# Kernel tuning notes

Hardware: AMD Instinct MI355X
Metric: run time of the kernel (lower is better)

The kernel has to match this reference:

```python
import jax, jax.numpy as jnp
import numpy as np

EMBED_DIM = 1024
NUM_HEADS = 16
HEAD_DIM = EMBED_DIM // NUM_HEADS


def setup_inputs() -> dict:
    key = jax.random.key(0)
    k_x, k_wqkv, k_bqkv, k_wout, k_bout = jax.random.split(key, 5)
    B, T, C = 4, 2048, EMBED_DIM
    bound_qkv = 1.0 / np.sqrt(C)
    bound_out = 1.0 / np.sqrt(C)
    return {
        "x": jax.random.normal(k_x, (B, T, C), dtype=jnp.float32),
        # nn.Linear stores weight as [out, in]; we keep that convention.
        "w_qkv": jax.random.uniform(k_wqkv, (3 * C, C), jnp.float32, -bound_qkv, bound_qkv),
        "b_qkv": jax.random.uniform(k_bqkv, (3 * C,), jnp.float32, -bound_qkv, bound_qkv),
        "w_out": jax.random.uniform(k_wout, (C, C), jnp.float32, -bound_out, bound_out),
        "b_out": jax.random.uniform(k_bout, (C,), jnp.float32, -bound_out, bound_out),
    }


def reference(x, w_qkv, b_qkv, w_out, b_out):
    B, T, C = x.shape
    H, D = NUM_HEADS, HEAD_DIM
    qkv = x @ w_qkv.T + b_qkv                     # [B, T, 3C]
    qkv = qkv.reshape(B, T, 3, H, D)
    q = jnp.transpose(qkv[:, :, 0], (0, 2, 1, 3))  # [B, H, T, D]
    k = jnp.transpose(qkv[:, :, 1], (0, 2, 1, 3))
    v = jnp.transpose(qkv[:, :, 2], (0, 2, 1, 3))
    att = jnp.einsum('bhqd,bhkd->bhqk', q, k) / jnp.sqrt(jnp.float32(D))
    causal = jnp.tril(jnp.ones((T, T), dtype=bool))
    att = jnp.where(causal[None, None], att, -jnp.inf)
    att = jax.nn.softmax(att, axis=-1)
    # dropout p=0.0 (eval-mode identity)
    out = jnp.einsum('bhqk,bhkd->bhqd', att, v)    # [B, H, T, D]
    out = jnp.transpose(out, (0, 2, 1, 3)).reshape(B, T, C)
    return out @ w_out.T + b_out
```

## Files before the change

### kernel.cpp

```cpp
#include <hip/hip_runtime.h>
#include <hip/hip_bf16.h>


#define B_ 4
#define T_ 2048
#define C_ 1024
#define H_ 16
#define D_ 64
#define M_ (B_*T_)

#define SCALE_LOG2 0.18033688f

typedef __attribute__((ext_vector_type(8))) short short8;
typedef __attribute__((ext_vector_type(4))) float f32x4;
typedef __attribute__((ext_vector_type(16))) float f32x16;

static __device__ __forceinline__ ushort f2bf(float f) {
  __hip_bfloat16 b = __float2bfloat16(f);
  ushort u; __builtin_memcpy(&u, &b, 2); return u;
}

static __device__ __forceinline__ void ld16(const void* g, void* l) {
  __builtin_amdgcn_global_load_lds((const __attribute__((address_space(1))) void*)g,
                                   (__attribute__((address_space(3))) void*)l, 16, 0, 0);
}

static __device__ __forceinline__ f32x4 mfma16(short8 a, short8 b, f32x4 c) {
  return __builtin_amdgcn_mfma_f32_16x16x32_bf16(a, b, c, 0, 0, 0);
}
static __device__ __forceinline__ f32x16 mfma32(short8 a, short8 b, f32x16 c) {
  return __builtin_amdgcn_mfma_f32_32x32x16_bf16(a, b, c, 0, 0, 0);
}

static __device__ __forceinline__ float pair_max(float x) {
  return fmaxf(x, __shfl_xor(x, 32));
}
static __device__ __forceinline__ float pair_sum(float x) {
  return x + __shfl_xor(x, 32);
}

__global__ void cvt_bf16(const float* __restrict__ in, ushort* __restrict__ out, int n4) {
  int i = blockIdx.x * blockDim.x + threadIdx.x;
  int st = gridDim.x * blockDim.x;
  for (; i < n4; i += st) {
    float4 v = ((const float4*)in)[i];
    ushort4 o;
    o.x = f2bf(v.x); o.y = f2bf(v.y); o.z = f2bf(v.z); o.w = f2bf(v.w);
    ((ushort4*)out)[i] = o;
  }
}

template<int MODE>
__global__ __launch_bounds__(256) void gemm_bt(
    const ushort* __restrict__ A, const ushort* __restrict__ Bm,
    const float* __restrict__ bias, int K,
    ushort* __restrict__ q, ushort* __restrict__ kk, ushort* __restrict__ vt,
    float* __restrict__ outF)
{
  __shared__ ushort Al[2][128*32];
  __shared__ ushort Bl[2][128*32];
  const int tid = threadIdx.x;
  const int lane = tid & 63;
  const int w = tid >> 6;
  const int wr = w >> 1, wc = w & 1;
  const int l15 = lane & 15, lhi = lane >> 4;
  const long i0 = (long)blockIdx.y * 128;
  const long j0 = (long)blockIdx.x * 128;

  const int gsw = (lhi ^ ((l15 >> 1) & 3)) * 8;

  auto STAGE = [&](int buf, int k0) {
    int c = tid;
    int row = c >> 2, gs = (c & 3) ^ ((row >> 1) & 3);
    ld16((const char*)A  + ((i0 + row) * K + k0 + gs * 8) * 2, (char*)&Al[buf][0] + c * 16);
    ld16((const char*)Bm + ((j0 + row) * K + k0 + gs * 8) * 2, (char*)&Bl[buf][0] + c * 16);
    c = tid + 256;
    row = c >> 2; gs = (c & 3) ^ ((row >> 1) & 3);
    ld16((const char*)A  + ((i0 + row) * K + k0 + gs * 8) * 2, (char*)&Al[buf][0] + c * 16);
    ld16((const char*)Bm + ((j0 + row) * K + k0 + gs * 8) * 2, (char*)&Bl[buf][0] + c * 16);
  };

  f32x4 acc[4][4] = {};
  const int nsteps = K >> 5;

  STAGE(0, 0);
  STAGE(1, 32);
  int cur = 0;

  for (int t = 0; t < nsteps; t++) {
    if (t + 1 < nsteps) { asm volatile("s_waitcnt vmcnt(4)" ::: "memory"); }
    else                { asm volatile("s_waitcnt vmcnt(0)" ::: "memory"); }
    __builtin_amdgcn_s_barrier();
    __builtin_amdgcn_sched_barrier(0);

    short8 af[4], bf[4];
#pragma unroll
    for (int m = 0; m < 4; m++) af[m] = *(const short8*)&Al[cur][(wr*64 + m*16 + l15)*32 + gsw];
#pragma unroll
    for (int n = 0; n < 4; n++) bf[n] = *(const short8*)&Bl[cur][(wc*64 + n*16 + l15)*32 + gsw];
    __builtin_amdgcn_s_setprio(1);
#pragma unroll
    for (int m = 0; m < 4; m++)
#pragma unroll
      for (int n = 0; n < 4; n++)
        acc[m][n] = mfma16(af[m], bf[n], acc[m][n]);
    __builtin_amdgcn_s_setprio(0);

    __builtin_amdgcn_s_barrier();
    __builtin_amdgcn_sched_barrier(0);
    if (t + 2 < nsteps) STAGE(cur, (t + 2) * 32);
    cur ^= 1;
  }

#pragma unroll
  for (int m = 0; m < 4; m++) {
#pragma unroll
    for (int n = 0; n < 4; n++) {
#pragma unroll
      for (int r = 0; r < 4; r++) {
        long i = i0 + wr*64 + m*16 + lhi*4 + r;
        int  j = (int)j0 + wc*64 + n*16 + l15;
        float v = acc[m][n][r] + bias[j];
        if (MODE == 0) {
          int b = (int)(i >> 11), t = (int)(i & 2047);
          int sel = j >> 10, cc = j & 1023;
          int h = cc >> 6, d = cc & 63;
          long bh = (long)b * H_ + h;
          if (sel == 0)      q [(bh*T_ + t)*D_ + d] = f2bf(v * SCALE_LOG2);
          else if (sel == 1) kk[(bh*T_ + t)*D_ + d] = f2bf(v);
          else               vt[(bh*D_ + d)*T_ + t] = f2bf(v);
        } else {
          outF[i * C_ + j] = v;
        }
      }
    }
  }
}

#define PSTR 20

static __device__ __forceinline__ void softmax_pack32(
    f32x16& sc, float& m, float& lp, f32x16 (&o)[2],
    int q0, int kvbase, int l31, int hi, uint* __restrict__ P)
{
  float sv[16];
  const bool needmask = (kvbase + 31 > q0);
#pragma unroll
  for (int r = 0; r < 16; r++) {
    float xv = sc[r];
    if (needmask) {
      int kv = kvbase + (r & 3) + 8 * (r >> 2) + 4 * hi;
      if (kv > q0 + l31) xv = -1e30f;
    }
    sv[r] = xv;
  }
  float p0 = fmaxf(fmaxf(sv[0], sv[1]),  fmaxf(sv[2], sv[3]));
  float p1 = fmaxf(fmaxf(sv[4], sv[5]),  fmaxf(sv[6], sv[7]));
  float p2 = fmaxf(fmaxf(sv[8], sv[9]),  fmaxf(sv[10], sv[11]));
  float p3 = fmaxf(fmaxf(sv[12], sv[13]), fmaxf(sv[14], sv[15]));
  float pm = fmaxf(fmaxf(p0, p1), fmaxf(p2, p3));
  float rowm = pair_max(pm);
  float nm = fmaxf(m, rowm);
  float alpha = __builtin_amdgcn_exp2f(m - nm);
  m = nm;
  lp *= alpha;
#pragma unroll
  for (int dt = 0; dt < 2; dt++)
#pragma unroll
    for (int r = 0; r < 16; r++) o[dt][r] *= alpha;
  float s = 0.f;
#pragma unroll
  for (int r = 0; r < 16; r++) {
    float p = __builtin_amdgcn_exp2f(sv[r] - m);
    sv[r] = p;
    s += p;
  }
  lp += s;
  uint W[8];
#pragma unroll
  for (int r = 0; r < 8; r++)
    asm("v_cvt_pk_bf16_f32 %0, %1, %2" : "=v"(W[r]) : "v"(sv[2*r]), "v"(sv[2*r+1]));
#pragma unroll
  for (int r2 = 0; r2 < 4; r2++) {
    uint2 pr; pr.x = W[2*r2]; pr.y = W[2*r2 + 1];
    *(uint2*)&P[l31 * PSTR + r2*4 + 2*hi] = pr;
  }
}

__global__ __launch_bounds__(256, 2) void attn_k(
    const ushort* __restrict__ Q, const ushort* __restrict__ K,
    const ushort* __restrict__ V, ushort* __restrict__ AO)
{
  __shared__ ushort Kt[2][128*64];
  __shared__ ushort Vt[2][64*128];
  __shared__ uint P2[4][32 * PSTR];
  const int tid = threadIdx.x;
  const int lane = tid & 63;
  const int w = tid >> 6;
  const int l31 = lane & 31, hi = lane >> 5;
  const int bb = blockIdx.x;
  const int head = bb & 63;
  const int i = bb >> 6;
  const int J = (i < 4) ? i : 11 - i;
  const int nst = 16 - J;
  const int q0a = 128 * J + 32 * w;
  const int q0b = 2016 - 128 * J - 32 * w;

  const ushort* Qb = Q + (size_t)head * T_ * D_;
  const ushort* Kb = K + (size_t)head * T_ * D_;
  const ushort* Vb = V + (size_t)head * D_ * T_;

  auto STAGE = [&](int buf, int kv0s) {
#pragma unroll
    for (int hb = 0; hb < 4; hb++) {
      int slot = tid + hb * 256;
      int krow = slot >> 3, kg = slot & 7, kgs = kg ^ (krow & 7);
      ld16((const char*)Kb + ((size_t)(kv0s + krow) * D_ + kgs * 8) * 2,
           (char*)&Kt[buf][0] + slot * 16);
      int vrow = slot >> 4, vg = slot & 15, vgs = vg ^ (vrow & 15);
      ld16((const char*)Vb + ((size_t)vrow * T_ + kv0s + vgs * 8) * 2,
           (char*)&Vt[buf][0] + slot * 16);
    }
  };

  short8 qfa[4], qfb[4];
#pragma unroll
  for (int s = 0; s < 4; s++) {
    qfa[s] = *(const short8*)&Qb[(q0a + l31) * D_ + s*16 + hi*8];
    qfb[s] = *(const short8*)&Qb[(q0b + l31) * D_ + s*16 + hi*8];
  }

  f32x16 oa[2] = {}, ob[2] = {};
  float ma = -1e30f, la = 0.f, mb = -1e30f, lb = 0.f;

  STAGE(0, 0);
  STAGE(1, 128);
  int cur = 0;
  uint* P = &P2[w][0];

  for (int t = 0; t < nst; t++) {
    const int kv0 = t * 128;
    if (t + 1 < nst) { asm volatile("s_waitcnt vmcnt(8)" ::: "memory"); }
    else             { asm volatile("s_waitcnt vmcnt(0)" ::: "memory"); }
    __builtin_amdgcn_s_barrier();
    __builtin_amdgcn_sched_barrier(0);

#pragma unroll
    for (int c = 0; c < 4; c++) {
      const int kvc = kv0 + 32 * c;
      const bool act_b = (kvc <= q0b + 31);
      const bool act_a = (kvc <= q0a + 31);
      if (act_b) {
        short8 kf[4];
#pragma unroll
        for (int s = 0; s < 4; s++) {
          const int row = c*32 + l31;
          kf[s] = *(const short8*)&Kt[cur][row*64 + (((2*s + hi) ^ (row & 7)) << 3)];
        }
        short8 vf[2][2];
#pragma unroll
        for (int sl = 0; sl < 2; sl++)
#pragma unroll
          for (int dt = 0; dt < 2; dt++) {
            const int row = dt*32 + l31;
            const int u = c*4 + sl*2 + hi;
            vf[sl][dt] = *(const short8*)
                &Vt[cur][row*128 + ((u ^ (row & 15)) << 3)];
          }

        {
          f32x16 scb = {};
          __builtin_amdgcn_s_setprio(1);
#pragma unroll
          for (int s = 0; s < 4; s++) scb = mfma32(kf[s], qfb[s], scb);
          __builtin_amdgcn_s_setprio(0);
          softmax_pack32(scb, mb, lb, ob, q0b, kvc, l31, hi, P);
          asm volatile("s_waitcnt lgkmcnt(0)" ::: "memory");
          __builtin_amdgcn_sched_barrier(0);
          short8 pf[2];
#pragma unroll
          for (int sl = 0; sl < 2; sl++) {
            uint4 pw = *(const uint4*)&P[l31 * PSTR + sl*8 + hi*4];
            __builtin_memcpy(&pf[sl], &pw, 16);
          }
          __builtin_amdgcn_s_setprio(1);
#pragma unroll
          for (int sl = 0; sl < 2; sl++)
#pragma unroll
            for (int dt = 0; dt < 2; dt++)
              ob[dt] = mfma32(vf[sl][dt], pf[sl], ob[dt]);
          __builtin_amdgcn_s_setprio(0);
          __builtin_amdgcn_sched_barrier(0);
        }
        if (act_a) {
          f32x16 sca = {};
          __builtin_amdgcn_s_setprio(1);
#pragma unroll
          for (int s = 0; s < 4; s++) sca = mfma32(kf[s], qfa[s], sca);
          __builtin_amdgcn_s_setprio(0);
          softmax_pack32(sca, ma, la, oa, q0a, kvc, l31, hi, P);
          asm volatile("s_waitcnt lgkmcnt(0)" ::: "memory");
          __builtin_amdgcn_sched_barrier(0);
          short8 pf[2];
#pragma unroll
          for (int sl = 0; sl < 2; sl++) {
            uint4 pw = *(const uint4*)&P[l31 * PSTR + sl*8 + hi*4];
            __builtin_memcpy(&pf[sl], &pw, 16);
          }
          __builtin_amdgcn_s_setprio(1);
#pragma unroll
          for (int sl = 0; sl < 2; sl++)
#pragma unroll
            for (int dt = 0; dt < 2; dt++)
              oa[dt] = mfma32(vf[sl][dt], pf[sl], oa[dt]);
          __builtin_amdgcn_s_setprio(0);
          __builtin_amdgcn_sched_barrier(0);
        }
      }
    }

    __builtin_amdgcn_s_barrier();
    __builtin_amdgcn_sched_barrier(0);
    if (t + 2 < nst) STAGE(cur, kv0 + 256);
    cur ^= 1;
  }

  const int b = head >> 4, h = head & 15;
  {
    const float invl = 1.0f / pair_sum(lb);
    const size_t rowb = (size_t)(b * T_ + q0b + l31) * C_ + h * 64;
#pragma unroll
    for (int dt = 0; dt < 2; dt++)
#pragma unroll
      for (int rg = 0; rg < 4; rg++) {
        const int d0 = dt*32 + 8*rg + 4*hi;
        ushort4 ov;
        ov.x = f2bf(ob[dt][rg*4+0] * invl);
        ov.y = f2bf(ob[dt][rg*4+1] * invl);
        ov.z = f2bf(ob[dt][rg*4+2] * invl);
        ov.w = f2bf(ob[dt][rg*4+3] * invl);
        *(ushort4*)&AO[rowb + d0] = ov;
      }
  }
  {
    const float invl = 1.0f / pair_sum(la);
    const size_t rowb = (size_t)(b * T_ + q0a + l31) * C_ + h * 64;
#pragma unroll
    for (int dt = 0; dt < 2; dt++)
#pragma unroll
      for (int rg = 0; rg < 4; rg++) {
        const int d0 = dt*32 + 8*rg + 4*hi;
        ushort4 ov;
        ov.x = f2bf(oa[dt][rg*4+0] * invl);
        ov.y = f2bf(oa[dt][rg*4+1] * invl);
        ov.z = f2bf(oa[dt][rg*4+2] * invl);
        ov.w = f2bf(oa[dt][rg*4+3] * invl);
        *(ushort4*)&AO[rowb + d0] = ov;
      }
  }
}

extern "C" void kernel_launch(void* const* d_in, const int* in_sizes, int n_in,
                              void* d_out, int out_size, void* d_ws, size_t ws_size,
                              hipStream_t stream) {
  const float* x     = (const float*)d_in[0];
  const float* w_qkv = (const float*)d_in[1];
  const float* b_qkv = (const float*)d_in[2];
  const float* w_out = (const float*)d_in[3];
  const float* b_out = (const float*)d_in[4];
  float* out = (float*)d_out;

  ushort* xb    = (ushort*)d_ws;
  ushort* wqkvb = xb    + (size_t)M_ * C_;
  ushort* woutb = wqkvb + (size_t)3 * C_ * C_;
  ushort* q     = woutb + (size_t)C_ * C_;
  ushort* kk    = q     + (size_t)M_ * C_;
  ushort* vt    = kk    + (size_t)M_ * C_;
  ushort* ao    = xb;

  cvt_bf16<<<1024, 256, 0, stream>>>(x,     xb,    (M_ * C_) / 4);
  cvt_bf16<<<512,  256, 0, stream>>>(w_qkv, wqkvb, (3 * C_ * C_) / 4);
  cvt_bf16<<<256,  256, 0, stream>>>(w_out, woutb, (C_ * C_) / 4);

  gemm_bt<0><<<dim3(3 * C_ / 128, M_ / 128), 256, 0, stream>>>(
      xb, wqkvb, b_qkv, C_, q, kk, vt, nullptr);

  attn_k<<<B_ * H_ * T_ / 256, 256, 0, stream>>>(q, kk, vt, ao);

  gemm_bt<1><<<dim3(C_ / 128, M_ / 128), 256, 0, stream>>>(
      ao, woutb, b_out, C_, nullptr, nullptr, nullptr, out);
}
```

Before: 206.5 us.

## Fuse conversion kernels, stage V-transpose epilogue via LDS, split attention blocks by row

After: 184.6 us. -10.6%, faster.

```diff
diff --git a/kernel.cpp b/kernel.cpp
--- a/kernel.cpp
+++ b/kernel.cpp
@@ -39,14 +39,22 @@
   return x + __shfl_xor(x, 32);
 }
 
-__global__ void cvt_bf16(const float* __restrict__ in, ushort* __restrict__ out, int n4) {
+__global__ void cvt3(const float* __restrict__ a, const float* __restrict__ b,
+                     const float* __restrict__ c, ushort* __restrict__ oa,
+                     ushort* __restrict__ ob, ushort* __restrict__ oc,
+                     int na, int nb, int nc) {
+  int tot = na + nb + nc;
   int i = blockIdx.x * blockDim.x + threadIdx.x;
   int st = gridDim.x * blockDim.x;
-  for (; i < n4; i += st) {
-    float4 v = ((const float4*)in)[i];
+  for (; i < tot; i += st) {
+    const float* s; ushort* d; int k = i;
+    if (k < na)            { s = a; d = oa; }
+    else if (k < na + nb)  { k -= na; s = b; d = ob; }
+    else                   { k -= na + nb; s = c; d = oc; }
+    float4 v = ((const float4*)s)[k];
     ushort4 o;
     o.x = f2bf(v.x); o.y = f2bf(v.y); o.z = f2bf(v.z); o.w = f2bf(v.w);
-    ((ushort4*)out)[i] = o;
+    ((ushort4*)d)[k] = o;
   }
 }
 
@@ -57,8 +65,7 @@
     ushort* __restrict__ q, ushort* __restrict__ kk, ushort* __restrict__ vt,
     float* __restrict__ outF)
 {
-  __shared__ ushort Al[2][128*32];
-  __shared__ ushort Bl[2][128*32];
+  __shared__ ushort SM[17408];
   const int tid = threadIdx.x;
   const int lane = tid & 63;
   const int w = tid >> 6;
@@ -72,12 +79,12 @@
   auto STAGE = [&](int buf, int k0) {
     int c = tid;
     int row = c >> 2, gs = (c & 3) ^ ((row >> 1) & 3);
-    ld16((const char*)A  + ((i0 + row) * K + k0 + gs * 8) * 2, (char*)&Al[buf][0] + c * 16);
-    ld16((const char*)Bm + ((j0 + row) * K + k0 + gs * 8) * 2, (char*)&Bl[buf][0] + c * 16);
+    ld16((const char*)A  + ((i0 + row) * K + k0 + gs * 8) * 2, (char*)SM + buf*8192 + c*16);
+    ld16((const char*)Bm + ((j0 + row) * K + k0 + gs * 8) * 2, (char*)SM + 16384 + buf*8192 + c*16);
     c = tid + 256;
     row = c >> 2; gs = (c & 3) ^ ((row >> 1) & 3);
-    ld16((const char*)A  + ((i0 + row) * K + k0 + gs * 8) * 2, (char*)&Al[buf][0] + c * 16);
-    ld16((const char*)Bm + ((j0 + row) * K + k0 + gs * 8) * 2, (char*)&Bl[buf][0] + c * 16);
+    ld16((const char*)A  + ((i0 + row) * K + k0 + gs * 8) * 2, (char*)SM + buf*8192 + c*16);
+    ld16((const char*)Bm + ((j0 + row) * K + k0 + gs * 8) * 2, (char*)SM + 16384 + buf*8192 + c*16);
   };
 
   f32x4 acc[4][4] = {};
@@ -95,9 +102,11 @@
 
     short8 af[4], bf[4];
 #pragma unroll
-    for (int m = 0; m < 4; m++) af[m] = *(const short8*)&Al[cur][(wr*64 + m*16 + l15)*32 + gsw];
-#pragma unroll
-    for (int n = 0; n < 4; n++) bf[n] = *(const short8*)&Bl[cur][(wc*64 + n*16 + l15)*32 + gsw];
+    for (int m = 0; m < 4; m++)
+      af[m] = *(const short8*)&SM[cur*4096 + (wr*64 + m*16 + l15)*32 + gsw];
+#pragma unroll
+    for (int n = 0; n < 4; n++)
+      bf[n] = *(const short8*)&SM[8192 + cur*4096 + (wc*64 + n*16 + l15)*32 + gsw];
     __builtin_amdgcn_s_setprio(1);
 #pragma unroll
     for (int m = 0; m < 4; m++)
@@ -112,25 +121,55 @@
     cur ^= 1;
   }
 
-#pragma unroll
-  for (int m = 0; m < 4; m++) {
-#pragma unroll
-    for (int n = 0; n < 4; n++) {
-#pragma unroll
-      for (int r = 0; r < 4; r++) {
-        long i = i0 + wr*64 + m*16 + lhi*4 + r;
-        int  j = (int)j0 + wc*64 + n*16 + l15;
-        float v = acc[m][n][r] + bias[j];
-        if (MODE == 0) {
-          int b = (int)(i >> 11), t = (int)(i & 2047);
-          int sel = j >> 10, cc = j & 1023;
-          int h = cc >> 6, d = cc & 63;
-          long bh = (long)b * H_ + h;
-          if (sel == 0)      q [(bh*T_ + t)*D_ + d] = f2bf(v * SCALE_LOG2);
-          else if (sel == 1) kk[(bh*T_ + t)*D_ + d] = f2bf(v);
-          else               vt[(bh*D_ + d)*T_ + t] = f2bf(v);
-        } else {
-          outF[i * C_ + j] = v;
+  if (MODE == 0 && j0 >= 2048) {
+#pragma unroll
+    for (int m = 0; m < 4; m++)
+#pragma unroll
+      for (int n = 0; n < 4; n++) {
+        const int jl = wc*64 + n*16 + l15;
+        const int tl = wr*64 + m*16 + lhi*4;
+        const float bs = bias[j0 + jl];
+        uint w0, w1;
+        asm("v_cvt_pk_bf16_f32 %0, %1, %2" : "=v"(w0)
+            : "v"(acc[m][n][0] + bs), "v"(acc[m][n][1] + bs));
+        asm("v_cvt_pk_bf16_f32 %0, %1, %2" : "=v"(w1)
+            : "v"(acc[m][n][2] + bs), "v"(acc[m][n][3] + bs));
+        uint2 pr; pr.x = w0; pr.y = w1;
+        *(uint2*)&SM[jl * 136 + tl] = pr;
+      }
+    __syncthreads();
+    const int b = (int)(i0 >> 11);
+    const int tb = (int)(i0 & 2047);
+#pragma unroll
+    for (int k2 = 0; k2 < 8; k2++) {
+      const int chunk = k2 * 256 + tid;
+      const int jl = chunk >> 4;
+      const int t0 = (chunk & 15) * 8;
+      uint4 pw = *(const uint4*)&SM[jl * 136 + t0];
+      const int cc = (int)((j0 + jl) & 1023);
+      const int h = cc >> 6, d = cc & 63;
+      *(uint4*)&vt[((size_t)(b * H_ + h) * D_ + d) * T_ + tb + t0] = pw;
+    }
+  } else {
+#pragma unroll
+    for (int m = 0; m < 4; m++) {
+#pragma unroll
+      for (int n = 0; n < 4; n++) {
+#pragma unroll
+        for (int r = 0; r < 4; r++) {
+          long i = i0 + wr*64 + m*16 + lhi*4 + r;
+          int  j = (int)j0 + wc*64 + n*16 + l15;
+          float v = acc[m][n][r] + bias[j];
+          if (MODE == 0) {
+            int b = (int)(i >> 11), t = (int)(i & 2047);
+            int cc = j & 1023;
+            int h = cc >> 6, d = cc & 63;
+            long bh = (long)b * H_ + h;
+            if (j < 1024)      q [(bh*T_ + t)*D_ + d] = f2bf(v * SCALE_LOG2);
+            else               kk[(bh*T_ + t)*D_ + d] = f2bf(v);
+          } else {
+            outF[i * C_ + j] = v;
+          }
         }
       }
     }
@@ -200,11 +239,9 @@
   const int l31 = lane & 31, hi = lane >> 5;
   const int bb = blockIdx.x;
   const int head = bb & 63;
-  const int i = bb >> 6;
-  const int J = (i < 4) ? i : 11 - i;
-  const int nst = 16 - J;
-  const int q0a = 128 * J + 32 * w;
-  const int q0b = 2016 - 128 * J - 32 * w;
+  const int rblk = 15 - (bb >> 6);
+  const int nst = rblk + 1;
+  const int q0 = 128 * rblk + 32 * w;
 
   const ushort* Qb = Q + (size_t)head * T_ * D_;
   const ushort* Kb = K + (size_t)head * T_ * D_;
@@ -223,15 +260,13 @@
     }
   };
 
-  short8 qfa[4], qfb[4];
-#pragma unroll
-  for (int s = 0; s < 4; s++) {
-    qfa[s] = *(const short8*)&Qb[(q0a + l31) * D_ + s*16 + hi*8];
-    qfb[s] = *(const short8*)&Qb[(q0b + l31) * D_ + s*16 + hi*8];
-  }
-
-  f32x16 oa[2] = {}, ob[2] = {};
-  float ma = -1e30f, la = 0.f, mb = -1e30f, lb = 0.f;
+  short8 qf[4];
+#pragma unroll
+  for (int s = 0; s < 4; s++)
+    qf[s] = *(const short8*)&Qb[(q0 + l31) * D_ + s*16 + hi*8];
+
+  f32x16 o[2] = {};
+  float m = -1e30f, lp = 0.f;
 
   STAGE(0, 0);
   STAGE(1, 128);
@@ -248,9 +283,7 @@
 #pragma unroll
     for (int c = 0; c < 4; c++) {
       const int kvc = kv0 + 32 * c;
-      const bool act_b = (kvc <= q0b + 31);
-      const bool act_a = (kvc <= q0a + 31);
-      if (act_b) {
+      if (kvc <= q0 + 31) {
         short8 kf[4];
 #pragma unroll
         for (int s = 0; s < 4; s++) {
@@ -268,54 +301,28 @@
                 &Vt[cur][row*128 + ((u ^ (row & 15)) << 3)];
           }
 
-        {
-          f32x16 scb = {};
-          __builtin_amdgcn_s_setprio(1);
-#pragma unroll
-          for (int s = 0; s < 4; s++) scb = mfma32(kf[s], qfb[s], scb);
-          __builtin_amdgcn_s_setprio(0);
-          softmax_pack32(scb, mb, lb, ob, q0b, kvc, l31, hi, P);
-          asm volatile("s_waitcnt lgkmcnt(0)" ::: "memory");
-          __builtin_amdgcn_sched_barrier(0);
-          short8 pf[2];
-#pragma unroll
-          for (int sl = 0; sl < 2; sl++) {
-            uint4 pw = *(const uint4*)&P[l31 * PSTR + sl*8 + hi*4];
-            __builtin_memcpy(&pf[sl], &pw, 16);
-          }
-          __builtin_amdgcn_s_setprio(1);
-#pragma unroll
-          for (int sl = 0; sl < 2; sl++)
-#pragma unroll
-            for (int dt = 0; dt < 2; dt++)
-              ob[dt] = mfma32(vf[sl][dt], pf[sl], ob[dt]);
-          __builtin_amdgcn_s_setprio(0);
-          __builtin_amdgcn_sched_barrier(0);
+        f32x16 sc = {};
+        __builtin_amdgcn_s_setprio(1);
+#pragma unroll
+        for (int s = 0; s < 4; s++) sc = mfma32(kf[s], qf[s], sc);
+        __builtin_amdgcn_s_setprio(0);
+        softmax_pack32(sc, m, lp, o, q0, kvc, l31, hi, P);
+        asm volatile("s_waitcnt lgkmcnt(0)" ::: "memory");
+        __builtin_amdgcn_sched_barrier(0);
+        short8 pf[2];
+#pragma unroll
+        for (int sl = 0; sl < 2; sl++) {
+          uint4 pw = *(const uint4*)&P[l31 * PSTR + sl*8 + hi*4];
+          __builtin_memcpy(&pf[sl], &pw, 16);
         }
-        if (act_a) {
-          f32x16 sca = {};
-          __builtin_amdgcn_s_setprio(1);
-#pragma unroll
-          for (int s = 0; s < 4; s++) sca = mfma32(kf[s], qfa[s], sca);
-          __builtin_amdgcn_s_setprio(0);
-          softmax_pack32(sca, ma, la, oa, q0a, kvc, l31, hi, P);
-          asm volatile("s_waitcnt lgkmcnt(0)" ::: "memory");
-          __builtin_amdgcn_sched_barrier(0);
-          short8 pf[2];
-#pragma unroll
-          for (int sl = 0; sl < 2; sl++) {
-            uint4 pw = *(const uint4*)&P[l31 * PSTR + sl*8 + hi*4];
-            __builtin_memcpy(&pf[sl], &pw, 16);
-          }
-          __builtin_amdgcn_s_setprio(1);
-#pragma unroll
-          for (int sl = 0; sl < 2; sl++)
-#pragma unroll
-            for (int dt = 0; dt < 2; dt++)
-              oa[dt] = mfma32(vf[sl][dt], pf[sl], oa[dt]);
-          __builtin_amdgcn_s_setprio(0);
-          __builtin_amdgcn_sched_barrier(0);
-        }
+        __builtin_amdgcn_s_setprio(1);
+#pragma unroll
+        for (int sl = 0; sl < 2; sl++)
+#pragma unroll
+          for (int dt = 0; dt < 2; dt++)
+            o[dt] = mfma32(vf[sl][dt], pf[sl], o[dt]);
+        __builtin_amdgcn_s_setprio(0);
+        __builtin_amdgcn_sched_barrier(0);
       }
     }
 
@@ -326,38 +333,20 @@
   }
 
   const int b = head >> 4, h = head & 15;
-  {
-    const float invl = 1.0f / pair_sum(lb);
-    const size_t rowb = (size_t)(b * T_ + q0b + l31) * C_ + h * 64;
-#pragma unroll
-    for (int dt = 0; dt < 2; dt++)
-#pragma unroll
-      for (int rg = 0; rg < 4; rg++) {
-        const int d0 = dt*32 + 8*rg + 4*hi;
-        ushort4 ov;
-        ov.x = f2bf(ob[dt][rg*4+0] * invl);
-        ov.y = f2bf(ob[dt][rg*4+1] * invl);
-        ov.z = f2bf(ob[dt][rg*4+2] * invl);
-        ov.w = f2bf(ob[dt][rg*4+3] * invl);
-        *(ushort4*)&AO[rowb + d0] = ov;
-      }
-  }
-  {
-    const float invl = 1.0f / pair_sum(la);
-    const size_t rowb = (size_t)(b * T_ + q0a + l31) * C_ + h * 64;
-#pragma unroll
-    for (int dt = 0; dt < 2; dt++)
-#pragma unroll
-      for (int rg = 0; rg < 4; rg++) {
-        const int d0 = dt*32 + 8*rg + 4*hi;
-        ushort4 ov;
-        ov.x = f2bf(oa[dt][rg*4+0] * invl);
-        ov.y = f2bf(oa[dt][rg*4+1] * invl);
-        ov.z = f2bf(oa[dt][rg*4+2] * invl);
-        ov.w = f2bf(oa[dt][rg*4+3] * invl);
-        *(ushort4*)&AO[rowb + d0] = ov;
-      }
-  }
+  const float invl = 1.0f / pair_sum(lp);
+  const size_t rowb = (size_t)(b * T_ + q0 + l31) * C_ + h * 64;
+#pragma unroll
+  for (int dt = 0; dt < 2; dt++)
+#pragma unroll
+    for (int rg = 0; rg < 4; rg++) {
+      const int d0 = dt*32 + 8*rg + 4*hi;
+      ushort4 ov;
+      ov.x = f2bf(o[dt][rg*4+0] * invl);
+      ov.y = f2bf(o[dt][rg*4+1] * invl);
+      ov.z = f2bf(o[dt][rg*4+2] * invl);
+      ov.w = f2bf(o[dt][rg*4+3] * invl);
+      *(ushort4*)&AO[rowb + d0] = ov;
+    }
 }
 
 extern "C" void kernel_launch(void* const* d_in, const int* in_sizes, int n_in,
@@ -378,14 +367,13 @@
   ushort* vt    = kk    + (size_t)M_ * C_;
   ushort* ao    = xb;
 
-  cvt_bf16<<<1024, 256, 0, stream>>>(x,     xb,    (M_ * C_) / 4);
-  cvt_bf16<<<512,  256, 0, stream>>>(w_qkv, wqkvb, (3 * C_ * C_) / 4);
-  cvt_bf16<<<256,  256, 0, stream>>>(w_out, woutb, (C_ * C_) / 4);
+  cvt3<<<2048, 256, 0, stream>>>(x, w_qkv, w_out, xb, wqkvb, woutb,
+                                 (M_ * C_) / 4, (3 * C_ * C_) / 4, (C_ * C_) / 4);
 
   gemm_bt<0><<<dim3(3 * C_ / 128, M_ / 128), 256, 0, stream>>>(
       xb, wqkvb, b_qkv, C_, q, kk, vt, nullptr);
 
-  attn_k<<<B_ * H_ * T_ / 256, 256, 0, stream>>>(q, kk, vt, ao);
+  attn_k<<<B_ * H_ * T_ / 128, 256, 0, stream>>>(q, kk, vt, ao);
 
   gemm_bt<1><<<dim3(C_ / 128, M_ / 128), 256, 0, stream>>>(
       ao, woutb, b_out, C_, nullptr, nullptr, nullptr, out);
```

## Fuse conversions, stage V-transpose via LDS, lazy softmax rescale, smaller attention tiles

Applied to the files above, without the earlier changes.

Result: faster. 175.8 us (-14.9%).

```diff
diff --git a/kernel.cpp b/kernel.cpp
--- a/kernel.cpp
+++ b/kernel.cpp
@@ -39,14 +39,22 @@
   return x + __shfl_xor(x, 32);
 }
 
-__global__ void cvt_bf16(const float* __restrict__ in, ushort* __restrict__ out, int n4) {
+__global__ void cvt3(const float* __restrict__ a, const float* __restrict__ b,
+                     const float* __restrict__ c, ushort* __restrict__ oa,
+                     ushort* __restrict__ ob, ushort* __restrict__ oc,
+                     int na, int nb, int nc) {
+  int tot = na + nb + nc;
   int i = blockIdx.x * blockDim.x + threadIdx.x;
   int st = gridDim.x * blockDim.x;
-  for (; i < n4; i += st) {
-    float4 v = ((const float4*)in)[i];
+  for (; i < tot; i += st) {
+    const float* s; ushort* d; int k = i;
+    if (k < na)            { s = a; d = oa; }
+    else if (k < na + nb)  { k -= na; s = b; d = ob; }
+    else                   { k -= na + nb; s = c; d = oc; }
+    float4 v = ((const float4*)s)[k];
     ushort4 o;
     o.x = f2bf(v.x); o.y = f2bf(v.y); o.z = f2bf(v.z); o.w = f2bf(v.w);
-    ((ushort4*)out)[i] = o;
+    ((ushort4*)d)[k] = o;
   }
 }
 
@@ -57,8 +65,7 @@
     ushort* __restrict__ q, ushort* __restrict__ kk, ushort* __restrict__ vt,
     float* __restrict__ outF)
 {
-  __shared__ ushort Al[2][128*32];
-  __shared__ ushort Bl[2][128*32];
+  __shared__ ushort SM[17408];
   const int tid = threadIdx.x;
   const int lane = tid & 63;
   const int w = tid >> 6;
@@ -72,12 +79,12 @@
   auto STAGE = [&](int buf, int k0) {
     int c = tid;
     int row = c >> 2, gs = (c & 3) ^ ((row >> 1) & 3);
-    ld16((const char*)A  + ((i0 + row) * K + k0 + gs * 8) * 2, (char*)&Al[buf][0] + c * 16);
-    ld16((const char*)Bm + ((j0 + row) * K + k0 + gs * 8) * 2, (char*)&Bl[buf][0] + c * 16);
+    ld16((const char*)A  + ((i0 + row) * K + k0 + gs * 8) * 2, (char*)SM + buf*8192 + c*16);
+    ld16((const char*)Bm + ((j0 + row) * K + k0 + gs * 8) * 2, (char*)SM + 16384 + buf*8192 + c*16);
     c = tid + 256;
     row = c >> 2; gs = (c & 3) ^ ((row >> 1) & 3);
-    ld16((const char*)A  + ((i0 + row) * K + k0 + gs * 8) * 2, (char*)&Al[buf][0] + c * 16);
-    ld16((const char*)Bm + ((j0 + row) * K + k0 + gs * 8) * 2, (char*)&Bl[buf][0] + c * 16);
+    ld16((const char*)A  + ((i0 + row) * K + k0 + gs * 8) * 2, (char*)SM + buf*8192 + c*16);
+    ld16((const char*)Bm + ((j0 + row) * K + k0 + gs * 8) * 2, (char*)SM + 16384 + buf*8192 + c*16);
   };
 
   f32x4 acc[4][4] = {};
@@ -95,9 +102,11 @@
 
     short8 af[4], bf[4];
 #pragma unroll
-    for (int m = 0; m < 4; m++) af[m] = *(const short8*)&Al[cur][(wr*64 + m*16 + l15)*32 + gsw];
-#pragma unroll
-    for (int n = 0; n < 4; n++) bf[n] = *(const short8*)&Bl[cur][(wc*64 + n*16 + l15)*32 + gsw];
+    for (int m = 0; m < 4; m++)
+      af[m] = *(const short8*)&SM[cur*4096 + (wr*64 + m*16 + l15)*32 + gsw];
+#pragma unroll
+    for (int n = 0; n < 4; n++)
+      bf[n] = *(const short8*)&SM[8192 + cur*4096 + (wc*64 + n*16 + l15)*32 + gsw];
     __builtin_amdgcn_s_setprio(1);
 #pragma unroll
     for (int m = 0; m < 4; m++)
@@ -112,25 +121,55 @@
     cur ^= 1;
   }
 
-#pragma unroll
-  for (int m = 0; m < 4; m++) {
-#pragma unroll
-    for (int n = 0; n < 4; n++) {
-#pragma unroll
-      for (int r = 0; r < 4; r++) {
-        long i = i0 + wr*64 + m*16 + lhi*4 + r;
-        int  j = (int)j0 + wc*64 + n*16 + l15;
-        float v = acc[m][n][r] + bias[j];
-        if (MODE == 0) {
-          int b = (int)(i >> 11), t = (int)(i & 2047);
-          int sel = j >> 10, cc = j & 1023;
-          int h = cc >> 6, d = cc & 63;
-          long bh = (long)b * H_ + h;
-          if (sel == 0)      q [(bh*T_ + t)*D_ + d] = f2bf(v * SCALE_LOG2);
-          else if (sel == 1) kk[(bh*T_ + t)*D_ + d] = f2bf(v);
-          else               vt[(bh*D_ + d)*T_ + t] = f2bf(v);
-        } else {
-          outF[i * C_ + j] = v;
+  if (MODE == 0 && j0 >= 2048) {
+#pragma unroll
+    for (int m = 0; m < 4; m++)
+#pragma unroll
+      for (int n = 0; n < 4; n++) {
+        const int jl = wc*64 + n*16 + l15;
+        const int tl = wr*64 + m*16 + lhi*4;
+        const float bs = bias[j0 + jl];
+        uint w0, w1;
+        asm("v_cvt_pk_bf16_f32 %0, %1, %2" : "=v"(w0)
+            : "v"(acc[m][n][0] + bs), "v"(acc[m][n][1] + bs));
+        asm("v_cvt_pk_bf16_f32 %0, %1, %2" : "=v"(w1)
+            : "v"(acc[m][n][2] + bs), "v"(acc[m][n][3] + bs));
+        uint2 pr; pr.x = w0; pr.y = w1;
+        *(uint2*)&SM[jl * 136 + tl] = pr;
+      }
+    __syncthreads();
+    const int b = (int)(i0 >> 11);
+    const int tb = (int)(i0 & 2047);
+#pragma unroll
+    for (int k2 = 0; k2 < 8; k2++) {
+      const int chunk = k2 * 256 + tid;
+      const int jl = chunk >> 4;
+      const int t0 = (chunk & 15) * 8;
+      uint4 pw = *(const uint4*)&SM[jl * 136 + t0];
+      const int cc = (int)((j0 + jl) & 1023);
+      const int h = cc >> 6, d = cc & 63;
+      *(uint4*)&vt[((size_t)(b * H_ + h) * D_ + d) * T_ + tb + t0] = pw;
+    }
+  } else {
+#pragma unroll
+    for (int m = 0; m < 4; m++) {
+#pragma unroll
+      for (int n = 0; n < 4; n++) {
+#pragma unroll
+        for (int r = 0; r < 4; r++) {
+          long i = i0 + wr*64 + m*16 + lhi*4 + r;
+          int  j = (int)j0 + wc*64 + n*16 + l15;
+          float v = acc[m][n][r] + bias[j];
+          if (MODE == 0) {
+            int b = (int)(i >> 11), t = (int)(i & 2047);
+            int cc = j & 1023;
+            int h = cc >> 6, d = cc & 63;
+            long bh = (long)b * H_ + h;
+            if (j < 1024)      q [(bh*T_ + t)*D_ + d] = f2bf(v * SCALE_LOG2);
+            else               kk[(bh*T_ + t)*D_ + d] = f2bf(v);
+          } else {
+            outF[i * C_ + j] = v;
+          }
         }
       }
     }
@@ -143,6 +182,7 @@
     f32x16& sc, float& m, float& lp, f32x16 (&o)[2],
     int q0, int kvbase, int l31, int hi, uint* __restrict__ P)
 {
+  const int sx = ((l31 >> 3) & 3) << 2;
   float sv[16];
   const bool needmask = (kvbase + 31 > q0);
 #pragma unroll
@@ -154,20 +194,23 @@
     }
     sv[r] = xv;
   }
-  float p0 = fmaxf(fmaxf(sv[0], sv[1]),  fmaxf(sv[2], sv[3]));
-  float p1 = fmaxf(fmaxf(sv[4], sv[5]),  fmaxf(sv[6], sv[7]));
-  float p2 = fmaxf(fmaxf(sv[8], sv[9]),  fmaxf(sv[10], sv[11]));
-  float p3 = fmaxf(fmaxf(sv[12], sv[13]), fmaxf(sv[14], sv[15]));
-  float pm = fmaxf(fmaxf(p0, p1), fmaxf(p2, p3));
-  float rowm = pair_max(pm);
-  float nm = fmaxf(m, rowm);
-  float alpha = __builtin_amdgcn_exp2f(m - nm);
-  m = nm;
-  lp *= alpha;
-#pragma unroll
-  for (int dt = 0; dt < 2; dt++)
-#pragma unroll
-    for (int r = 0; r < 16; r++) o[dt][r] *= alpha;
+  float a0 = fmaxf(fmaxf(sv[0], sv[1]), sv[2]);
+  float a1 = fmaxf(fmaxf(sv[3], sv[4]), sv[5]);
+  float a2 = fmaxf(fmaxf(sv[6], sv[7]), sv[8]);
+  float a3 = fmaxf(fmaxf(sv[9], sv[10]), sv[11]);
+  float a4 = fmaxf(fmaxf(sv[12], sv[13]), sv[14]);
+  float pmax = fmaxf(fmaxf(fmaxf(a0, a1), a2), fmaxf(fmaxf(a3, a4), sv[15]));
+  if (__any(pmax > m + 8.0f)) {
+    float rowm = pair_max(pmax);
+    float nm = fmaxf(m, rowm);
+    float alpha = __builtin_amdgcn_exp2f(m - nm);
+    m = nm;
+    lp *= alpha;
+#pragma unroll
+    for (int dt = 0; dt < 2; dt++)
+#pragma unroll
+      for (int r = 0; r < 16; r++) o[dt][r] *= alpha;
+  }
   float s = 0.f;
 #pragma unroll
   for (int r = 0; r < 16; r++) {
@@ -183,7 +226,7 @@
 #pragma unroll
   for (int r2 = 0; r2 < 4; r2++) {
     uint2 pr; pr.x = W[2*r2]; pr.y = W[2*r2 + 1];
-    *(uint2*)&P[l31 * PSTR + r2*4 + 2*hi] = pr;
+    *(uint2*)&P[l31 * PSTR + ((r2*4) ^ sx) + 2*hi] = pr;
   }
 }
 
@@ -191,18 +234,19 @@
     const ushort* __restrict__ Q, const ushort* __restrict__ K,
     const ushort* __restrict__ V, ushort* __restrict__ AO)
 {
-  __shared__ ushort Kt[2][128*64];
-  __shared__ ushort Vt[2][64*128];
+  __shared__ ushort Kt[2][64*64];
+  __shared__ ushort Vt[2][64*64];
   __shared__ uint P2[4][32 * PSTR];
   const int tid = threadIdx.x;
   const int lane = tid & 63;
   const int w = tid >> 6;
   const int l31 = lane & 31, hi = lane >> 5;
+  const int sx = ((l31 >> 3) & 3) << 2;
   const int bb = blockIdx.x;
   const int head = bb & 63;
   const int i = bb >> 6;
   const int J = (i < 4) ? i : 11 - i;
-  const int nst = 16 - J;
+  const int nst = 32 - 2 * J;
   const int q0a = 128 * J + 32 * w;
   const int q0b = 2016 - 128 * J - 32 * w;
 
@@ -212,13 +256,12 @@
 
   auto STAGE = [&](int buf, int kv0s) {
 #pragma unroll
-    for (int hb = 0; hb < 4; hb++) {
+    for (int hb = 0; hb < 2; hb++) {
       int slot = tid + hb * 256;
-      int krow = slot >> 3, kg = slot & 7, kgs = kg ^ (krow & 7);
-      ld16((const char*)Kb + ((size_t)(kv0s + krow) * D_ + kgs * 8) * 2,
+      int row = slot >> 3, g = slot & 7, gs = g ^ (row & 7);
+      ld16((const char*)Kb + ((size_t)(kv0s + row) * D_ + gs * 8) * 2,
            (char*)&Kt[buf][0] + slot * 16);
-      int vrow = slot >> 4, vg = slot & 15, vgs = vg ^ (vrow & 15);
-      ld16((const char*)Vb + ((size_t)vrow * T_ + kv0s + vgs * 8) * 2,
+      ld16((const char*)Vb + ((size_t)row * T_ + kv0s + gs * 8) * 2,
            (char*)&Vt[buf][0] + slot * 16);
     }
   };
@@ -234,19 +277,19 @@
   float ma = -1e30f, la = 0.f, mb = -1e30f, lb = 0.f;
 
   STAGE(0, 0);
-  STAGE(1, 128);
+  STAGE(1, 64);
   int cur = 0;
   uint* P = &P2[w][0];
 
   for (int t = 0; t < nst; t++) {
-    const int kv0 = t * 128;
-    if (t + 1 < nst) { asm volatile("s_waitcnt vmcnt(8)" ::: "memory"); }
+    const int kv0 = t * 64;
+    if (t + 1 < nst) { asm volatile("s_waitcnt vmcnt(4)" ::: "memory"); }
     else             { asm volatile("s_waitcnt vmcnt(0)" ::: "memory"); }
     __builtin_amdgcn_s_barrier();
     __builtin_amdgcn_sched_barrier(0);
 
 #pragma unroll
-    for (int c = 0; c < 4; c++) {
+    for (int c = 0; c < 2; c++) {
       const int kvc = kv0 + 32 * c;
       const bool act_b = (kvc <= q0b + 31);
       const bool act_a = (kvc <= q0a + 31);
@@ -264,8 +307,7 @@
           for (int dt = 0; dt < 2; dt++) {
             const int row = dt*32 + l31;
             const int u = c*4 + sl*2 + hi;
-            vf[sl][dt] = *(const short8*)
-                &Vt[cur][row*128 + ((u ^ (row & 15)) << 3)];
+            vf[sl][dt] = *(const short8*)&Vt[cur][row*64 + ((u ^ (row & 7)) << 3)];
           }
 
         {
@@ -280,7 +322,7 @@
           short8 pf[2];
 #pragma unroll
           for (int sl = 0; sl < 2; sl++) {
-            uint4 pw = *(const uint4*)&P[l31 * PSTR + sl*8 + hi*4];
+            uint4 pw = *(const uint4*)&P[l31 * PSTR + ((sl*8 + hi*4) ^ sx)];
             __builtin_memcpy(&pf[sl], &pw, 16);
           }
           __builtin_amdgcn_s_setprio(1);
@@ -304,7 +346,7 @@
           short8 pf[2];
 #pragma unroll
           for (int sl = 0; sl < 2; sl++) {
-            uint4 pw = *(const uint4*)&P[l31 * PSTR + sl*8 + hi*4];
+            uint4 pw = *(const uint4*)&P[l31 * PSTR + ((sl*8 + hi*4) ^ sx)];
             __builtin_memcpy(&pf[sl], &pw, 16);
           }
           __builtin_amdgcn_s_setprio(1);
@@ -321,7 +363,7 @@
 
     __builtin_amdgcn_s_barrier();
     __builtin_amdgcn_sched_barrier(0);
-    if (t + 2 < nst) STAGE(cur, kv0 + 256);
+    if (t + 2 < nst) STAGE(cur, kv0 + 128);
     cur ^= 1;
   }
 
@@ -378,9 +420,8 @@
   ushort* vt    = kk    + (size_t)M_ * C_;
   ushort* ao    = xb;
 
-  cvt_bf16<<<1024, 256, 0, stream>>>(x,     xb,    (M_ * C_) / 4);
-  cvt_bf16<<<512,  256, 0, stream>>>(w_qkv, wqkvb, (3 * C_ * C_) / 4);
-  cvt_bf16<<<256,  256, 0, stream>>>(w_out, woutb, (C_ * C_) / 4);
+  cvt3<<<2048, 256, 0, stream>>>(x, w_qkv, w_out, xb, wqkvb, woutb,
+                                 (M_ * C_) / 4, (3 * C_ * C_) / 4, (C_ * C_) / 4);
 
   gemm_bt<0><<<dim3(3 * C_ / 128, M_ / 128), 256, 0, stream>>>(
       xb, wqkvb, b_qkv, C_, q, kk, vt, nullptr);
```
